# Optimization experiments

Hardware: AMD Instinct MI355X
Metric: run time of the kernel (lower is better)

Reference implementation:

```python
import jax, jax.numpy as jnp
import numpy as np

N_NODES = 100000
N_EDGES = 1600000
EDGE_FEAT = 16
EDGE_HID = 32
NODE_FEAT = 128


def setup_inputs() -> dict:
    key = jax.random.key(0)
    ks = jax.random.split(key, 10)
    inp = {
        "edge_logits": jax.random.normal(ks[0], (N_EDGES, 1), dtype=jnp.float32),
        "edge_feats": jax.random.normal(ks[1], (N_EDGES, EDGE_FEAT), dtype=jnp.float32),
        "node_feats": jax.random.normal(ks[2], (N_NODES, NODE_FEAT), dtype=jnp.float32),
        "dst": jax.random.randint(ks[3], (N_EDGES,), 0, N_NODES, dtype=jnp.int32),
        # edge_transform Linear(edge_feat -> edge_hid)
        "W_et": jax.random.normal(ks[4], (EDGE_FEAT, EDGE_HID), dtype=jnp.float32) * (1.0 / np.sqrt(EDGE_FEAT)),
        "b_et": jnp.zeros((EDGE_HID,), dtype=jnp.float32),
        # MLP Linear(edge_hid + node_feat -> node_feat)
        "W1": jax.random.normal(ks[5], (EDGE_HID + NODE_FEAT, NODE_FEAT), dtype=jnp.float32) * (1.0 / np.sqrt(EDGE_HID + NODE_FEAT)),
        "b1": jnp.zeros((NODE_FEAT,), dtype=jnp.float32),
        # MLP Linear(node_feat -> node_feat)
        "W2": jax.random.normal(ks[6], (NODE_FEAT, NODE_FEAT), dtype=jnp.float32) * (1.0 / np.sqrt(NODE_FEAT)),
        "b2": jnp.zeros((NODE_FEAT,), dtype=jnp.float32),
    }
    return inp


def reference(edge_logits, edge_feats, node_feats, dst, W_et, b_et, W1, b1, W2, b2):
    # edge_softmax: segment softmax of edge_logits grouped by destination node
    logits = edge_logits[:, 0]                                        # [E]
    seg_max = jax.ops.segment_max(logits, dst, num_segments=N_NODES)  # [N]
    seg_max = jnp.where(jnp.isfinite(seg_max), seg_max, 0.0)          # guard empty segments
    ex = jnp.exp(logits - seg_max[dst])                               # [E]
    denom = jax.ops.segment_sum(ex, dst, num_segments=N_NODES)        # [N]
    denom = jnp.where(denom == 0.0, 1.0, denom)
    alpha = ex / denom[dst]                                           # [E]
    # edge transform (dropout is identity in eval) then weight by attention
    e = alpha[:, None] * (edge_feats @ W_et + b_et)                   # [E, H]
    # scatter-sum aggregation to destination nodes
    c = jax.ops.segment_sum(e, dst, num_segments=N_NODES)             # [N, H]
    context = jax.nn.elu(c)
    h = jnp.concatenate([context, node_feats], axis=1)                # [N, H+F]
    h = jax.nn.relu(h @ W1 + b1)
    return jax.nn.relu(h @ W2 + b2)                                   # [N, F]
```

## Files before the change

### kernel.cpp

```cpp
#include <hip/hip_runtime.h>

#define EF 16
#define EH 32
#define NF 128
#define K1 160
#define HS 168
#define H2S 136
#define CW 16

typedef __attribute__((ext_vector_type(8))) short bf16x8;
typedef __attribute__((ext_vector_type(4))) float f32x4;

__device__ __forceinline__ unsigned short f2b(float f) {
  unsigned u = __float_as_uint(f);
  u += 0x7FFFu + ((u >> 16) & 1u);
  return (unsigned short)(u >> 16);
}
__device__ __forceinline__ unsigned pack2b(float a, float b) {
  return (unsigned)f2b(a) | ((unsigned)f2b(b) << 16);
}
__device__ __forceinline__ void atom_pk_bf16(unsigned* addr, unsigned val) {
  asm volatile("global_atomic_pk_add_bf16 %0, %1, off" :: "v"(addr), "v"(val) : "memory");
}

__global__ void k_init(unsigned* __restrict__ ctxd, int n,
                       const float* __restrict__ W1, const float* __restrict__ W2,
                       unsigned short* __restrict__ w1t, unsigned short* __restrict__ w2t) {
  int i = blockIdx.x * blockDim.x + threadIdx.x;
  if (i < n * CW) ctxd[i] = 0u;
  if (i < K1 * NF) {
    int nn = i / K1, k = i % K1;
    w1t[i] = f2b(W1[k * NF + nn]);
  } else if (i < K1 * NF + NF * NF) {
    int j = i - K1 * NF;
    int nn = j / NF, k = j % NF;
    w2t[j] = f2b(W2[k * NF + nn]);
  }
}

__global__ __launch_bounds__(256) void k_edge(
    const int* __restrict__ dst, const float* __restrict__ logits,
    const float* __restrict__ efeat,
    unsigned* __restrict__ ctxd, int n_edges) {
  int gid = (int)((blockIdx.x * blockDim.x + threadIdx.x) >> 3);
  int c = threadIdx.x & 7;
  int ngroups = (int)((gridDim.x * blockDim.x) >> 3);
#pragma unroll 2
  for (int e = gid; e < n_edges; e += ngroups) {
    int d = dst[e];
    float ex = __expf(logits[e]);
    float2 f = *(const float2*)&efeat[(size_t)e * EF + c * 2];
    unsigned* row = &ctxd[(size_t)d * CW];
    atom_pk_bf16(row + c, pack2b(ex * f.x, ex * f.y));
    if (c == 0) unsafeAtomicAdd((float*)(row + 8), ex);
  }
}

__global__ __launch_bounds__(256) void k_node(
    const unsigned* __restrict__ ctxd,
    const float* __restrict__ W_et, const float* __restrict__ b_et,
    const float* __restrict__ nf,
    const unsigned short* __restrict__ w1t, const unsigned short* __restrict__ w2t,
    const float* __restrict__ b1, const float* __restrict__ b2,
    float* __restrict__ out, int n_nodes) {
  __shared__ __align__(16) unsigned short hA[64 * HS];
  __shared__ __align__(16) unsigned short hB[64 * H2S];
  const int t = threadIdx.x;
  const int w = t >> 6, lane = t & 63;
  const int m = lane & 15, q = lane >> 4;
  int n0 = blockIdx.x * 64;
  if (n0 + 64 > n_nodes) n0 = n_nodes - 64;

  {
    int node = t >> 2, jg = (t & 3) * 8;
    const unsigned* row = &ctxd[(size_t)(n0 + node) * CW];
    float den = __uint_as_float(row[8]);
    float inv = (den > 0.0f) ? 1.0f / den : 0.0f;
    float S = (den > 0.0f) ? 1.0f : 0.0f;
    const unsigned short* cr = (const unsigned short*)row;
    float cf[EF];
#pragma unroll
    for (int k = 0; k < EF; ++k) cf[k] = __uint_as_float((unsigned)cr[k] << 16);
    unsigned short r[8];
#pragma unroll
    for (int jj = 0; jj < 8; ++jj) {
      int j = jg + jj;
      float acc = 0.0f;
#pragma unroll
      for (int k = 0; k < EF; ++k) acc += cf[k] * W_et[k * EH + j];
      float cv = acc * inv + S * b_et[j];
      float ctxv = (cv > 0.0f) ? cv : (__expf(cv) - 1.0f);
      r[jj] = f2b(ctxv);
    }
    *(uint4*)&hA[node * HS + jg] = *(const uint4*)r;
  }
#pragma unroll
  for (int i = 0; i < 8; ++i) {
    int idx = t + 256 * i;
    int node = idx >> 5, j = (idx & 31) * 4;
    float4 v = *(const float4*)&nf[(size_t)(n0 + node) * NF + j];
    unsigned short r[4] = {f2b(v.x), f2b(v.y), f2b(v.z), f2b(v.w)};
    *(uint2*)&hA[node * HS + EH + j] = *(const uint2*)r;
  }
  __syncthreads();

  const int mr = w * 16;
  f32x4 acc[8];
#pragma unroll
  for (int nt = 0; nt < 8; ++nt) acc[nt] = (f32x4){0.f, 0.f, 0.f, 0.f};
  for (int ks = 0; ks < 5; ++ks) {
    bf16x8 a = *(const bf16x8*)&hA[(mr + m) * HS + ks * 32 + q * 8];
#pragma unroll
    for (int nt = 0; nt < 8; ++nt) {
      bf16x8 b = *(const bf16x8*)&w1t[(size_t)(nt * 16 + m) * K1 + ks * 32 + q * 8];
      acc[nt] = __builtin_amdgcn_mfma_f32_16x16x32_bf16(a, b, acc[nt], 0, 0, 0);
    }
  }
#pragma unroll
  for (int nt = 0; nt < 8; ++nt) {
    float bb = b1[nt * 16 + m];
#pragma unroll
    for (int r = 0; r < 4; ++r) {
      float v = fmaxf(acc[nt][r] + bb, 0.0f);
      hB[(mr + q * 4 + r) * H2S + nt * 16 + m] = f2b(v);
    }
  }
  __syncthreads();

  f32x4 ac2[8];
#pragma unroll
  for (int nt = 0; nt < 8; ++nt) ac2[nt] = (f32x4){0.f, 0.f, 0.f, 0.f};
  for (int ks = 0; ks < 4; ++ks) {
    bf16x8 a = *(const bf16x8*)&hB[(mr + m) * H2S + ks * 32 + q * 8];
#pragma unroll
    for (int nt = 0; nt < 8; ++nt) {
      bf16x8 b = *(const bf16x8*)&w2t[(size_t)(nt * 16 + m) * NF + ks * 32 + q * 8];
      ac2[nt] = __builtin_amdgcn_mfma_f32_16x16x32_bf16(a, b, ac2[nt], 0, 0, 0);
    }
  }
#pragma unroll
  for (int nt = 0; nt < 8; ++nt) {
    float bb = b2[nt * 16 + m];
#pragma unroll
    for (int r = 0; r < 4; ++r) {
      out[(size_t)(n0 + mr + q * 4 + r) * NF + nt * 16 + m] = fmaxf(ac2[nt][r] + bb, 0.0f);
    }
  }
}

extern "C" void kernel_launch(void* const* d_in, const int* in_sizes, int n_in,
                              void* d_out, int out_size, void* d_ws, size_t ws_size,
                              hipStream_t stream) {
  const float* edge_logits = (const float*)d_in[0];
  const float* edge_feats  = (const float*)d_in[1];
  const float* node_feats  = (const float*)d_in[2];
  const int*   dst         = (const int*)d_in[3];
  const float* W_et        = (const float*)d_in[4];
  const float* b_et        = (const float*)d_in[5];
  const float* W1          = (const float*)d_in[6];
  const float* b1          = (const float*)d_in[7];
  const float* W2          = (const float*)d_in[8];
  const float* b2          = (const float*)d_in[9];
  float* out = (float*)d_out;

  const int E = in_sizes[0];
  const int n = in_sizes[2] / NF;

  unsigned* ctxd = (unsigned*)(((uintptr_t)d_ws + 63) & ~(uintptr_t)63);
  unsigned short* w1t = (unsigned short*)(ctxd + (size_t)n * CW);
  unsigned short* w2t = w1t + NF * K1;

  const int thr = 256;
  const int initN = n * CW;

  k_init<<<(initN + thr - 1) / thr, thr, 0, stream>>>(ctxd, n, W1, W2, w1t, w2t);
  k_edge<<<2048, thr, 0, stream>>>(dst, edge_logits, edge_feats, ctxd, E);
  k_node<<<(n + 63) / 64, 256, 0, stream>>>(ctxd, W_et, b_et, node_feats,
                                            w1t, w2t, b1, b2, out, n);
}
```

Before: 390.3 us.

## Stage W_et and output tile through LDS, vectorize ctx loads, coalesce output stores

```diff
diff --git a/kernel.cpp b/kernel.cpp
--- a/kernel.cpp
+++ b/kernel.cpp
@@ -7,6 +7,7 @@
 #define HS 168
 #define H2S 136
 #define CW 16
+#define OBS 132
 
 typedef __attribute__((ext_vector_type(8))) short bf16x8;
 typedef __attribute__((ext_vector_type(4))) float f32x4;
@@ -63,37 +64,19 @@
     const unsigned short* __restrict__ w1t, const unsigned short* __restrict__ w2t,
     const float* __restrict__ b1, const float* __restrict__ b2,
     float* __restrict__ out, int n_nodes) {
-  __shared__ __align__(16) unsigned short hA[64 * HS];
-  __shared__ __align__(16) unsigned short hB[64 * H2S];
+  __shared__ __align__(16) unsigned char smem[40960];
+  unsigned short* hA = (unsigned short*)smem;
+  unsigned short* hB = (unsigned short*)(smem + 21504);
+  float* wet = (float*)(smem + 38912);
+  float* obuf = (float*)smem;
   const int t = threadIdx.x;
   const int w = t >> 6, lane = t & 63;
   const int m = lane & 15, q = lane >> 4;
   int n0 = blockIdx.x * 64;
   if (n0 + 64 > n_nodes) n0 = n_nodes - 64;
 
-  {
-    int node = t >> 2, jg = (t & 3) * 8;
-    const unsigned* row = &ctxd[(size_t)(n0 + node) * CW];
-    float den = __uint_as_float(row[8]);
-    float inv = (den > 0.0f) ? 1.0f / den : 0.0f;
-    float S = (den > 0.0f) ? 1.0f : 0.0f;
-    const unsigned short* cr = (const unsigned short*)row;
-    float cf[EF];
-#pragma unroll
-    for (int k = 0; k < EF; ++k) cf[k] = __uint_as_float((unsigned)cr[k] << 16);
-    unsigned short r[8];
-#pragma unroll
-    for (int jj = 0; jj < 8; ++jj) {
-      int j = jg + jj;
-      float acc = 0.0f;
-#pragma unroll
-      for (int k = 0; k < EF; ++k) acc += cf[k] * W_et[k * EH + j];
-      float cv = acc * inv + S * b_et[j];
-      float ctxv = (cv > 0.0f) ? cv : (__expf(cv) - 1.0f);
-      r[jj] = f2b(ctxv);
-    }
-    *(uint4*)&hA[node * HS + jg] = *(const uint4*)r;
-  }
+  wet[t] = W_et[t];
+  wet[t + 256] = W_et[t + 256];
 #pragma unroll
   for (int i = 0; i < 8; ++i) {
     int idx = t + 256 * i;
@@ -104,6 +87,38 @@
   }
   __syncthreads();
 
+  {
+    int node = t >> 2, jg = (t & 3) * 8;
+    const unsigned* row = &ctxd[(size_t)(n0 + node) * CW];
+    uint4 va = *(const uint4*)row;
+    uint4 vb = *(const uint4*)(row + 4);
+    float den = __uint_as_float(row[8]);
+    float inv = (den > 0.0f) ? 1.0f / den : 0.0f;
+    float S = (den > 0.0f) ? 1.0f : 0.0f;
+    float cf[EF];
+    {
+      unsigned wd[8] = {va.x, va.y, va.z, va.w, vb.x, vb.y, vb.z, vb.w};
+#pragma unroll
+      for (int p = 0; p < 8; ++p) {
+        cf[2 * p]     = __uint_as_float(wd[p] << 16);
+        cf[2 * p + 1] = __uint_as_float(wd[p] & 0xFFFF0000u);
+      }
+    }
+    unsigned short r[8];
+#pragma unroll
+    for (int jj = 0; jj < 8; ++jj) {
+      int j = jg + jj;
+      float acc = 0.0f;
+#pragma unroll
+      for (int k = 0; k < EF; ++k) acc += cf[k] * wet[k * EH + j];
+      float cv = acc * inv + S * b_et[j];
+      float ctxv = (cv > 0.0f) ? cv : (__expf(cv) - 1.0f);
+      r[jj] = f2b(ctxv);
+    }
+    *(uint4*)&hA[node * HS + jg] = *(const uint4*)r;
+  }
+  __syncthreads();
+
   const int mr = w * 16;
   f32x4 acc[8];
 #pragma unroll
@@ -138,13 +153,24 @@
       ac2[nt] = __builtin_amdgcn_mfma_f32_16x16x32_bf16(a, b, ac2[nt], 0, 0, 0);
     }
   }
+  __syncthreads();
+
 #pragma unroll
   for (int nt = 0; nt < 8; ++nt) {
     float bb = b2[nt * 16 + m];
 #pragma unroll
     for (int r = 0; r < 4; ++r) {
-      out[(size_t)(n0 + mr + q * 4 + r) * NF + nt * 16 + m] = fmaxf(ac2[nt][r] + bb, 0.0f);
-    }
+      obuf[(mr + q * 4 + r) * OBS + nt * 16 + m] = fmaxf(ac2[nt][r] + bb, 0.0f);
+    }
+  }
+  __syncthreads();
+
+#pragma unroll
+  for (int i = 0; i < 8; ++i) {
+    int f = t + 256 * i;
+    int row = f >> 5, jf = (f & 31) * 4;
+    f32x4 v = *(const f32x4*)&obuf[row * OBS + jf];
+    __builtin_nontemporal_store(v, (f32x4*)&out[(size_t)(n0 + row) * NF + jf]);
   }
 }
 
```

Result: slower. 402.9 us (+3.2%).
